# Kernel optimization log

Measured on AMD Instinct MI355X. Metric: run time of the kernel, lower is better.

## Reference

```python
import jax, jax.numpy as jnp
import numpy as np

B, S, D = 2, 2048, 1024
H, DK = 16, 64          # heads, d_k (= d_v)
DH = 4096               # FFN hidden
EPS = 1e-5


def _layer_norm(x, gamma, beta):
    mu = jnp.mean(x, axis=-1, keepdims=True)
    var = jnp.var(x, axis=-1, keepdims=True)
    return (x - mu) * jax.lax.rsqrt(var + EPS) * gamma + beta


def setup_inputs() -> dict:
    key = jax.random.key(0)
    ks = jax.random.split(key, 8)
    s = lambda fan_in: 1.0 / np.sqrt(fan_in)
    return {
        "x": jax.random.normal(ks[0], (B, S, D), dtype=jnp.float32),
        # NOTE: source module uses W_q for queries, keys AND values (bug kept faithfully),
        # so W_k / W_v are never used and are not materialized.
        "Wq": jax.random.normal(ks[1], (D, H * DK), dtype=jnp.float32) * s(D),
        "bq": jnp.zeros((H * DK,), dtype=jnp.float32),
        "Wo": jax.random.normal(ks[2], (H * DK, D), dtype=jnp.float32) * s(H * DK),
        "bo": jnp.zeros((D,), dtype=jnp.float32),
        "ln1_g": jnp.ones((D,), dtype=jnp.float32),
        "ln1_b": jnp.zeros((D,), dtype=jnp.float32),
        "W1": jax.random.normal(ks[3], (D, DH), dtype=jnp.float32) * s(D),
        "b1": jnp.zeros((DH,), dtype=jnp.float32),
        "W2": jax.random.normal(ks[4], (DH, D), dtype=jnp.float32) * s(DH),
        "b2": jnp.zeros((D,), dtype=jnp.float32),
        "ln2_g": jnp.ones((D,), dtype=jnp.float32),
        "ln2_b": jnp.zeros((D,), dtype=jnp.float32),
    }


def reference(x, Wq, bq, Wo, bo, ln1_g, ln1_b, W1, b1, W2, b2, ln2_g, ln2_b):
    residual = x
    # projections: q, k, v all use W_q (faithful to source)
    q = (x @ Wq + bq).reshape(B, S, H, DK)
    k = (x @ Wq + bq).reshape(B, S, H, DK)
    v = (x @ Wq + bq).reshape(B, S, H, DK)
    # scores scaled by sqrt(sequence_length), as in the source
    scale = 1.0 / jnp.sqrt(jnp.float32(S))
    scores = jnp.einsum("bqhd,bkhd->bhqk", q, k) * scale
    probs = jax.nn.softmax(scores, axis=-1)
    attn = jnp.einsum("bhqk,bkhd->bqhd", probs, v).reshape(B, S, H * DK)
    attn = attn @ Wo + bo
    # dropout is identity in eval mode
    x = _layer_norm(attn + residual, ln1_g, ln1_b)
    residual = x
    h = jax.nn.relu(x @ W1 + b1)
    x = h @ W2 + b2
    x = _layer_norm(x + residual, ln2_g, ln2_b)
    return x
```

## Files before the change

kernel.cpp:

```cpp
#include <hip/hip_runtime.h>
#include <stdint.h>


typedef unsigned short u16;
typedef __attribute__((ext_vector_type(8))) short v8s;
typedef __attribute__((ext_vector_type(4))) float v4f;

#define AS1 __attribute__((address_space(1)))
#define AS3 __attribute__((address_space(3)))

__device__ __forceinline__ void gl_lds16(const u16* g, u16* l) {
  __builtin_amdgcn_global_load_lds((const AS1 void*)g, (AS3 void*)l, 16, 0, 0);
}

__device__ __forceinline__ float bf2f(u16 u) {
  union { uint32_t i; float f; } v; v.i = ((uint32_t)u) << 16; return v.f;
}
__device__ __forceinline__ u16 f2bf(float f) {
  union { float f; uint32_t i; } v; v.f = f;
  uint32_t x = v.i;
  return (u16)((x + 0x7FFFu + ((x >> 16) & 1u)) >> 16);
}
__device__ __forceinline__ uint32_t fbits(float f) {
  union { float f; uint32_t u; } v; v.f = f; return v.u;
}

__global__ __launch_bounds__(256) void cvt_f2b(
    const float* __restrict__ src, u16* __restrict__ dst, int n4) {
  int i = (blockIdx.x * 256 + threadIdx.x);
  if (i < n4) {
    float4 v = *(const float4*)(src + (size_t)i * 4);
    ushort4 o;
    o.x = f2bf(v.x); o.y = f2bf(v.y); o.z = f2bf(v.z); o.w = f2bf(v.w);
    *(ushort4*)(dst + (size_t)i * 4) = o;
  }
}

__global__ __launch_bounds__(256) void transpose_f2b(
    const float* __restrict__ src, u16* __restrict__ dst,
    int R, int C, int ld_s, int ld_d) {
  __shared__ float tile[32][33];
  const int tx = threadIdx.x & 31, ty = threadIdx.x >> 5;
  const int c0 = blockIdx.x * 32, r0 = blockIdx.y * 32;
#pragma unroll
  for (int j = 0; j < 32; j += 8)
    tile[ty + j][tx] = src[(size_t)(r0 + ty + j) * ld_s + c0 + tx];
  __syncthreads();
#pragma unroll
  for (int j = 0; j < 32; j += 8)
    dst[(size_t)(c0 + ty + j) * ld_d + r0 + tx] = f2bf(tile[tx][ty + j]);
}

__global__ __launch_bounds__(256) void transpose_b2b(
    const u16* __restrict__ src, u16* __restrict__ dst,
    int R, int C, int ld_s, int ld_d) {
  __shared__ u16 tile[32][33];
  const int tx = threadIdx.x & 31, ty = threadIdx.x >> 5;
  const int c0 = blockIdx.x * 32, r0 = blockIdx.y * 32;
#pragma unroll
  for (int j = 0; j < 32; j += 8)
    tile[ty + j][tx] = src[(size_t)(r0 + ty + j) * ld_s + c0 + tx];
  __syncthreads();
#pragma unroll
  for (int j = 0; j < 32; j += 8)
    dst[(size_t)(c0 + ty + j) * ld_d + r0 + tx] = tile[tx][ty + j];
}

__global__ __launch_bounds__(256) void gemm_g1(
    const u16* __restrict__ A, const u16* __restrict__ Bt,
    const float* __restrict__ bias, void* __restrict__ C,
    int M, int N, int ldk, int klen, int relu, int accum, int out_f32,
    int atomic) {
  __shared__ u16 As[2][4096];
  __shared__ u16 Bs[2][4096];
  const int tid = threadIdx.x;
  const int w = tid >> 6, l = tid & 63;
  const int lane16 = l & 15, kgrp = l >> 4;
  const int m0 = blockIdx.y * 128, n0 = blockIdx.x * 128;
  const int k_begin = blockIdx.z * klen;
  const int wr = (w >> 1) * 64, wc = (w & 1) * 64;

  const int sr = w * 32 + (l >> 2);
  const int sc = l & 3;
  const int sgc = sc ^ ((sr & 3) ^ ((sr >> 2) & 3));
  const u16* gA = A + (size_t)(m0 + sr) * ldk + k_begin + 8 * sgc;
  const u16* gB = Bt + (size_t)(n0 + sr) * ldk + k_begin + 8 * sgc;
  const size_t rstep = (size_t)16 * ldk;
  const int fl = (lane16 & 3) ^ ((lane16 >> 2) & 3);

  v4f acc[4][4];
#pragma unroll
  for (int i = 0; i < 4; i++)
#pragma unroll
    for (int j = 0; j < 4; j++)
#pragma unroll
      for (int r = 0; r < 4; r++) acc[i][j][r] = 0.f;

  gl_lds16(gA, &As[0][w * 1024]);
  gl_lds16(gA + rstep, &As[0][w * 1024 + 512]);
  gl_lds16(gB, &Bs[0][w * 1024]);
  gl_lds16(gB + rstep, &Bs[0][w * 1024 + 512]);

  int cur = 0;
  for (int k0 = 0; k0 < klen; k0 += 32) {
    __syncthreads();
    if (k0 + 32 < klen) {
      int nxt = cur ^ 1;
      gl_lds16(gA + k0 + 32, &As[nxt][w * 1024]);
      gl_lds16(gA + k0 + 32 + rstep, &As[nxt][w * 1024 + 512]);
      gl_lds16(gB + k0 + 32, &Bs[nxt][w * 1024]);
      gl_lds16(gB + k0 + 32 + rstep, &Bs[nxt][w * 1024 + 512]);
    }
    v8s a[4], b[4];
#pragma unroll
    for (int mi = 0; mi < 4; mi++)
      a[mi] = *(const v8s*)(&As[cur][(wr + mi * 16 + lane16) * 32 + 8 * (kgrp ^ fl)]);
#pragma unroll
    for (int ni = 0; ni < 4; ni++)
      b[ni] = *(const v8s*)(&Bs[cur][(wc + ni * 16 + lane16) * 32 + 8 * (kgrp ^ fl)]);
#pragma unroll
    for (int mi = 0; mi < 4; mi++)
#pragma unroll
      for (int ni = 0; ni < 4; ni++)
        acc[mi][ni] = __builtin_amdgcn_mfma_f32_16x16x32_bf16(a[mi], b[ni], acc[mi][ni], 0, 0, 0);
    cur ^= 1;
  }

#pragma unroll
  for (int ni = 0; ni < 4; ni++) {
    int col = n0 + wc + ni * 16 + lane16;
    float bv = (bias && k_begin == 0) ? bias[col] : 0.f;
#pragma unroll
    for (int mi = 0; mi < 4; mi++) {
      int row = m0 + wr + mi * 16 + kgrp * 4;
#pragma unroll
      for (int r = 0; r < 4; r++) {
        float v = acc[mi][ni][r] + bv;
        if (relu) v = fmaxf(v, 0.f);
        size_t idx = (size_t)(row + r) * N + col;
        if (atomic) {
          atomicAdd(&((float*)C)[idx], v);
        } else if (out_f32) {
          float* Cf = (float*)C;
          if (accum) v += Cf[idx];
          Cf[idx] = v;
        } else {
          ((u16*)C)[idx] = f2bf(v);
        }
      }
    }
  }
}

__global__ __launch_bounds__(256) void gemm_g2(
    const u16* __restrict__ A, const u16* __restrict__ Bt,
    const float* __restrict__ bias, void* __restrict__ C,
    int M, int N, int K, int relu, int accum, int out_f32) {
  __shared__ u16 As[2][8192];
  __shared__ u16 Bs[2][4096];
  const int tid = threadIdx.x;
  const int w = tid >> 6, l = tid & 63;
  const int l16 = l & 15, kgrp = l >> 4;
  const int m0 = blockIdx.y * 128, n0 = blockIdx.x * 64;
  const int wr = (w >> 1) * 64, wc = (w & 1) * 32;

  const int srow = w * 8 + (l >> 3);
  const u16* gA[4];
#pragma unroll
  for (int i = 0; i < 4; i++) {
    int r = i * 32 + srow;
    gA[i] = A + (size_t)(m0 + r) * K + 8 * ((l & 7) ^ (r & 7));
  }
  const u16* gB[2];
#pragma unroll
  for (int i = 0; i < 2; i++) {
    int r = i * 32 + srow;
    gB[i] = Bt + (size_t)(n0 + r) * K + 8 * ((l & 7) ^ (r & 7));
  }

  v4f acc[4][2];
#pragma unroll
  for (int i = 0; i < 4; i++)
#pragma unroll
    for (int j = 0; j < 2; j++)
#pragma unroll
      for (int r = 0; r < 4; r++) acc[i][j][r] = 0.f;

#pragma unroll
  for (int i = 0; i < 4; i++) gl_lds16(gA[i], &As[0][(i * 256 + w * 64) * 8]);
#pragma unroll
  for (int i = 0; i < 2; i++) gl_lds16(gB[i], &Bs[0][(i * 256 + w * 64) * 8]);

  int cur = 0;
  for (int k0 = 0; k0 < K; k0 += 64) {
    __syncthreads();
    if (k0 + 64 < K) {
      int nxt = cur ^ 1;
#pragma unroll
      for (int i = 0; i < 4; i++)
        gl_lds16(gA[i] + k0 + 64, &As[nxt][(i * 256 + w * 64) * 8]);
#pragma unroll
      for (int i = 0; i < 2; i++)
        gl_lds16(gB[i] + k0 + 64, &Bs[nxt][(i * 256 + w * 64) * 8]);
    }
    v8s a[4][2], b[2][2];
#pragma unroll
    for (int ks = 0; ks < 2; ks++) {
      int ch = 8 * ((ks * 4 + kgrp) ^ (l16 & 7));
#pragma unroll
      for (int mi = 0; mi < 4; mi++)
        a[mi][ks] = *(const v8s*)(&As[cur][(wr + mi * 16 + l16) * 64 + ch]);
#pragma unroll
      for (int ni = 0; ni < 2; ni++)
        b[ni][ks] = *(const v8s*)(&Bs[cur][(wc + ni * 16 + l16) * 64 + ch]);
    }
#pragma unroll
    for (int ks = 0; ks < 2; ks++)
#pragma unroll
      for (int mi = 0; mi < 4; mi++)
#pragma unroll
        for (int ni = 0; ni < 2; ni++)
          acc[mi][ni] = __builtin_amdgcn_mfma_f32_16x16x32_bf16(a[mi][ks], b[ni][ks], acc[mi][ni], 0, 0, 0);
    cur ^= 1;
  }

#pragma unroll
  for (int ni = 0; ni < 2; ni++) {
    int col = n0 + wc + ni * 16 + l16;
    float bv = bias ? bias[col] : 0.f;
#pragma unroll
    for (int mi = 0; mi < 4; mi++) {
      int row = m0 + wr + mi * 16 + kgrp * 4;
#pragma unroll
      for (int r = 0; r < 4; r++) {
        float v = acc[mi][ni][r] + bv;
        if (relu) v = fmaxf(v, 0.f);
        size_t idx = (size_t)(row + r) * N + col;
        if (out_f32) {
          float* Cf = (float*)C;
          if (accum) v += Cf[idx];
          Cf[idx] = v;
        } else {
          ((u16*)C)[idx] = f2bf(v);
        }
      }
    }
  }
}

__global__ __launch_bounds__(256) void attn_kernel(
    const u16* __restrict__ Q, const u16* __restrict__ Qt,
    u16* __restrict__ O) {
  __shared__ u16 KV[2][8192];
  __shared__ __align__(16) u16 Ps[4][2304];
  const int tid = threadIdx.x;
  const int w = tid >> 6, l = tid & 63;
  const int l16 = l & 15, kgrp = l >> 4;
  const int bh = blockIdx.y, b = bh >> 4, h = bh & 15;
  const int q0 = blockIdx.x * 128;
  const size_t rowQ = (size_t)(b * 2048 + q0 + w * 32);
  const float cexp = 1.4426950408889634f / 45.254833995939045f;

  const int srow = w * 8 + (l >> 3);
  const int sch8 = 8 * ((l & 7) ^ (srow & 7));
  const u16* gK0 = Q + (size_t)(b * 2048 + srow) * 1024 + h * 64 + sch8;
  const u16* gK1 = gK0 + (size_t)32 * 1024;
  const u16* gV0 = Qt + (size_t)(h * 64 + srow) * 4096 + b * 2048 + sch8;
  const u16* gV1 = gV0 + (size_t)32 * 4096;

  v8s qb[2][2];
#pragma unroll
  for (int nj = 0; nj < 2; nj++)
#pragma unroll
    for (int ks = 0; ks < 2; ks++) {
      v8s t = *(const v8s*)(Q + (rowQ + nj * 16 + l16) * 1024 + h * 64 + ks * 32 + kgrp * 8);
#pragma unroll
      for (int j = 0; j < 8; j++) t[j] = (short)f2bf(bf2f((u16)t[j]) * cexp);
      qb[nj][ks] = t;
    }

  v4f o[2][4];
  float ls[2] = {0.f, 0.f};
#pragma unroll
  for (int i = 0; i < 2; i++)
#pragma unroll
    for (int j = 0; j < 4; j++)
#pragma unroll
      for (int r = 0; r < 4; r++) o[i][j][r] = 0.f;

  gl_lds16(gK0, &KV[0][w * 512]);
  gl_lds16(gK1, &KV[0][2048 + w * 512]);
  gl_lds16(gV0, &KV[0][4096 + w * 512]);
  gl_lds16(gV1, &KV[0][4096 + 2048 + w * 512]);

  u16* Pw = &Ps[w][0];
  int cur = 0;
  for (int kb = 0; kb < 2048; kb += 64) {
    __syncthreads();
    if (kb + 64 < 2048) {
      int nxt = cur ^ 1;
      gl_lds16(gK0 + (size_t)(kb + 64) * 1024, &KV[nxt][w * 512]);
      gl_lds16(gK1 + (size_t)(kb + 64) * 1024, &KV[nxt][2048 + w * 512]);
      gl_lds16(gV0 + (kb + 64), &KV[nxt][4096 + w * 512]);
      gl_lds16(gV1 + (kb + 64), &KV[nxt][4096 + 2048 + w * 512]);
    }
    const u16* Ks = &KV[cur][0];
    const u16* Vt = &KV[cur][4096];

    v4f st[4][2];
#pragma unroll
    for (int i = 0; i < 4; i++)
#pragma unroll
      for (int j = 0; j < 2; j++)
#pragma unroll
        for (int r = 0; r < 4; r++) st[i][j][r] = 0.f;
#pragma unroll
    for (int ks = 0; ks < 2; ks++) {
      v8s ka[4];
#pragma unroll
      for (int mi = 0; mi < 4; mi++)
        ka[mi] = *(const v8s*)(Ks + (mi * 16 + l16) * 64 + 8 * ((ks * 4 + kgrp) ^ (l16 & 7)));
#pragma unroll
      for (int mi = 0; mi < 4; mi++)
#pragma unroll
        for (int nj = 0; nj < 2; nj++)
          st[mi][nj] = __builtin_amdgcn_mfma_f32_16x16x32_bf16(ka[mi], qb[nj][ks], st[mi][nj], 0, 0, 0);
    }

#pragma unroll
    for (int mi = 0; mi < 4; mi++)
#pragma unroll
      for (int nj = 0; nj < 2; nj++) {
        float p0 = __builtin_amdgcn_exp2f(st[mi][nj][0]);
        float p1 = __builtin_amdgcn_exp2f(st[mi][nj][1]);
        float p2 = __builtin_amdgcn_exp2f(st[mi][nj][2]);
        float p3 = __builtin_amdgcn_exp2f(st[mi][nj][3]);
        ls[nj] += (p0 + p1) + (p2 + p3);
        uint2 pk;
        pk.x = __builtin_amdgcn_perm(fbits(p1), fbits(p0), 0x07060302u);
        pk.y = __builtin_amdgcn_perm(fbits(p3), fbits(p2), 0x07060302u);
        *(uint2*)(Pw + (nj * 16 + l16) * 72 + mi * 16 + kgrp * 4) = pk;
      }

#pragma unroll
    for (int t = 0; t < 2; t++) {
      v8s pa[2], vb[4];
#pragma unroll
      for (int nj = 0; nj < 2; nj++)
        pa[nj] = *(const v8s*)(Pw + (nj * 16 + l16) * 72 + t * 32 + kgrp * 8);
#pragma unroll
      for (int ni = 0; ni < 4; ni++)
        vb[ni] = *(const v8s*)(Vt + (ni * 16 + l16) * 64 + 8 * ((t * 4 + kgrp) ^ (l16 & 7)));
#pragma unroll
      for (int nj = 0; nj < 2; nj++)
#pragma unroll
        for (int ni = 0; ni < 4; ni++)
          o[nj][ni] = __builtin_amdgcn_mfma_f32_16x16x32_bf16(pa[nj], vb[ni], o[nj][ni], 0, 0, 0);
    }
    cur ^= 1;
  }

#pragma unroll
  for (int nj = 0; nj < 2; nj++) {
    float t = ls[nj];
    t += __shfl_xor(t, 16, 64);
    t += __shfl_xor(t, 32, 64);
    ls[nj] = t;
  }

#pragma unroll
  for (int nj = 0; nj < 2; nj++) {
#pragma unroll
    for (int r = 0; r < 4; r++) {
      float den = __shfl(ls[nj], kgrp * 4 + r, 64);
      float rden = 1.f / den;
#pragma unroll
      for (int ni = 0; ni < 4; ni++) {
        O[(rowQ + nj * 16 + kgrp * 4 + r) * 1024 + h * 64 + ni * 16 + l16] =
            f2bf(o[nj][ni][r] * rden);
      }
    }
  }
}

__global__ __launch_bounds__(256) void ln_residual(
    const void* __restrict__ Y, const void* __restrict__ Xr,
    const float* __restrict__ g, const float* __restrict__ bb,
    void* __restrict__ out, int yf, int xf, int of) {
  const int row = blockIdx.x, tid = threadIdx.x;
  const size_t base = (size_t)row * 1024;
  float v[4], s = 0.f, sq = 0.f;
#pragma unroll
  for (int i = 0; i < 4; i++) {
    int c = tid + i * 256;
    float ya = yf ? ((const float*)Y)[base + c] : bf2f(((const u16*)Y)[base + c]);
    float xa = xf ? ((const float*)Xr)[base + c] : bf2f(((const u16*)Xr)[base + c]);
    float x = ya + xa;
    v[i] = x; s += x; sq += x * x;
  }
#pragma unroll
  for (int off = 32; off >= 1; off >>= 1) {
    s += __shfl_down(s, off, 64);
    sq += __shfl_down(sq, off, 64);
  }
  __shared__ float rs[4], rq[4];
  const int w = tid >> 6, l = tid & 63;
  if (l == 0) { rs[w] = s; rq[w] = sq; }
  __syncthreads();
  s = rs[0] + rs[1] + rs[2] + rs[3];
  sq = rq[0] + rq[1] + rq[2] + rq[3];
  const float mu = s * (1.f / 1024.f);
  const float var = sq * (1.f / 1024.f) - mu * mu;
  const float rstd = rsqrtf(var + 1e-5f);
#pragma unroll
  for (int i = 0; i < 4; i++) {
    int c = tid + i * 256;
    float r = (v[i] - mu) * rstd * g[c] + bb[c];
    if (of) ((float*)out)[base + c] = r;
    else ((u16*)out)[base + c] = f2bf(r);
  }
}

extern "C" void kernel_launch(void* const* d_in, const int* in_sizes, int n_in,
                              void* d_out, int out_size, void* d_ws, size_t ws_size,
                              hipStream_t stream) {
  const float* x   = (const float*)d_in[0];
  const float* Wq  = (const float*)d_in[1];
  const float* bq  = (const float*)d_in[2];
  const float* Wo  = (const float*)d_in[3];
  const float* bo  = (const float*)d_in[4];
  const float* g1  = (const float*)d_in[5];
  const float* be1 = (const float*)d_in[6];
  const float* W1  = (const float*)d_in[7];
  const float* b1  = (const float*)d_in[8];
  const float* W2  = (const float*)d_in[9];
  const float* b2  = (const float*)d_in[10];
  const float* g2  = (const float*)d_in[11];
  const float* be2 = (const float*)d_in[12];
  float* out = (float*)d_out;
  u16* ws  = (u16*)d_ws;

  const size_t M1 = 1048576;
  dim3 blk(256);
  const bool big = ws_size >= (size_t)37 * M1 * 2;

  if (big) {
    u16* xb   = ws + 0;
    u16* Qb   = ws + 4 * M1;
    u16* Qt   = ws + 8 * M1;
    u16* WqT  = ws + 12 * M1;
    u16* W1T  = ws + 13 * M1;
    u16* W2T  = ws + 17 * M1;
    u16* Hh   = ws + 21 * M1;
    u16* attn = xb;  u16* Yb = Qt;  u16* x1 = Qb;  u16* WoT = WqT;

    hipMemsetAsync(out, 0, (size_t)out_size * sizeof(float), stream);

    cvt_f2b<<<dim3(4096), blk, 0, stream>>>(x, xb, 1048576);
    transpose_f2b<<<dim3(32, 32), blk, 0, stream>>>(Wq, WqT, 1024, 1024, 1024, 1024);
    gemm_g2<<<dim3(16, 32), blk, 0, stream>>>(xb, WqT, bq, Qb, 4096, 1024, 1024, 0, 0, 0);

    transpose_b2b<<<dim3(32, 128), blk, 0, stream>>>(Qb, Qt, 4096, 1024, 1024, 4096);
    attn_kernel<<<dim3(16, 32), blk, 0, stream>>>(Qb, Qt, attn);

    transpose_f2b<<<dim3(32, 32), blk, 0, stream>>>(Wo, WoT, 1024, 1024, 1024, 1024);
    gemm_g2<<<dim3(16, 32), blk, 0, stream>>>(attn, WoT, bo, Yb, 4096, 1024, 1024, 0, 0, 0);
    ln_residual<<<dim3(4096), blk, 0, stream>>>(Yb, x, g1, be1, x1, 0, 1, 0);

    transpose_f2b<<<dim3(128, 32), blk, 0, stream>>>(W1, W1T, 1024, 4096, 4096, 1024);
    gemm_g1<<<dim3(32, 32, 1), blk, 0, stream>>>(x1, W1T, b1, Hh, 4096, 4096,
                                                 1024, 1024, 1, 0, 0, 0);
    transpose_f2b<<<dim3(32, 128), blk, 0, stream>>>(W2, W2T, 4096, 1024, 1024, 4096);
    gemm_g1<<<dim3(8, 32, 4), blk, 0, stream>>>(Hh, W2T, b2, out, 4096, 1024,
                                                4096, 1024, 0, 0, 1, 1);

    ln_residual<<<dim3(4096), blk, 0, stream>>>(out, x1, g2, be2, out, 1, 0, 1);
  } else {
    u16* xb   = ws + 0;
    u16* Qb   = ws + 4 * M1;
    u16* Qt   = ws + 8 * M1;
    u16* attn = xb;  u16* Yb = Qt;  u16* x1 = Qb;  u16* Hc = xb;
    u16* Wt1  = ws + 12 * M1;
    u16* Wt2  = ws + 13 * M1;

    cvt_f2b<<<dim3(4096), blk, 0, stream>>>(x, xb, 1048576);
    transpose_f2b<<<dim3(32, 32), blk, 0, stream>>>(Wq, Wt1, 1024, 1024, 1024, 1024);
    gemm_g2<<<dim3(16, 32), blk, 0, stream>>>(xb, Wt1, bq, Qb, 4096, 1024, 1024, 0, 0, 0);

    transpose_b2b<<<dim3(32, 128), blk, 0, stream>>>(Qb, Qt, 4096, 1024, 1024, 4096);
    attn_kernel<<<dim3(16, 32), blk, 0, stream>>>(Qb, Qt, attn);

    transpose_f2b<<<dim3(32, 32), blk, 0, stream>>>(Wo, Wt2, 1024, 1024, 1024, 1024);
    gemm_g2<<<dim3(16, 32), blk, 0, stream>>>(attn, Wt2, bo, Yb, 4096, 1024, 1024, 0, 0, 0);
    ln_residual<<<dim3(4096), blk, 0, stream>>>(Yb, x, g1, be1, x1, 0, 1, 0);

    for (int c = 0; c < 4; c++) {
      transpose_f2b<<<dim3(32, 32), blk, 0, stream>>>(W1 + (size_t)c * 1024, Wt1,
                                                      1024, 1024, 4096, 1024);
      gemm_g2<<<dim3(16, 32), blk, 0, stream>>>(x1, Wt1, b1 + (size_t)c * 1024, Hc,
                                                4096, 1024, 1024, 1, 0, 0);
      transpose_f2b<<<dim3(32, 32), blk, 0, stream>>>(W2 + (size_t)c * M1, Wt2,
                                                      1024, 1024, 1024, 1024);
      gemm_g2<<<dim3(16, 32), blk, 0, stream>>>(Hc, Wt2, (c == 0) ? b2 : (const float*)nullptr,
                                                out, 4096, 1024, 1024, 0, (c > 0) ? 1 : 0, 1);
    }
    ln_residual<<<dim3(4096), blk, 0, stream>>>(out, x1, g2, be2, out, 1, 0, 1);
  }
}
```

Before: 391.4 us.

## Replace atomic split-K with two-way split-K partial buffers reduced in LayerNorm

Adds a split-K GEMM variant (gemm_g2s) that writes the first K-half to the main output and the second K-half as bf16 partials to a scratch buffer. The LayerNorm kernel now sums the two partials, which removes the memset and the fp32 atomicAdd reduction in the W2 GEMM. Split-K is also applied to the Wo projection to raise block count. The trade-off is extra partial-buffer traffic, and storing the second partial in bf16 costs some precision.

```diff
diff --git a/kernel.cpp b/kernel.cpp
--- a/kernel.cpp
+++ b/kernel.cpp
@@ -69,23 +69,21 @@
 __global__ __launch_bounds__(256) void gemm_g1(
     const u16* __restrict__ A, const u16* __restrict__ Bt,
     const float* __restrict__ bias, void* __restrict__ C,
-    int M, int N, int ldk, int klen, int relu, int accum, int out_f32,
-    int atomic) {
+    int M, int N, int K, int relu, int out_f32) {
   __shared__ u16 As[2][4096];
   __shared__ u16 Bs[2][4096];
   const int tid = threadIdx.x;
   const int w = tid >> 6, l = tid & 63;
   const int lane16 = l & 15, kgrp = l >> 4;
   const int m0 = blockIdx.y * 128, n0 = blockIdx.x * 128;
-  const int k_begin = blockIdx.z * klen;
   const int wr = (w >> 1) * 64, wc = (w & 1) * 64;
 
   const int sr = w * 32 + (l >> 2);
   const int sc = l & 3;
   const int sgc = sc ^ ((sr & 3) ^ ((sr >> 2) & 3));
-  const u16* gA = A + (size_t)(m0 + sr) * ldk + k_begin + 8 * sgc;
-  const u16* gB = Bt + (size_t)(n0 + sr) * ldk + k_begin + 8 * sgc;
-  const size_t rstep = (size_t)16 * ldk;
+  const u16* gA = A + (size_t)(m0 + sr) * K + 8 * sgc;
+  const u16* gB = Bt + (size_t)(n0 + sr) * K + 8 * sgc;
+  const size_t rstep = (size_t)16 * K;
   const int fl = (lane16 & 3) ^ ((lane16 >> 2) & 3);
 
   v4f acc[4][4];
@@ -102,9 +100,9 @@
   gl_lds16(gB + rstep, &Bs[0][w * 1024 + 512]);
 
   int cur = 0;
-  for (int k0 = 0; k0 < klen; k0 += 32) {
+  for (int k0 = 0; k0 < K; k0 += 32) {
     __syncthreads();
-    if (k0 + 32 < klen) {
+    if (k0 + 32 < K) {
       int nxt = cur ^ 1;
       gl_lds16(gA + k0 + 32, &As[nxt][w * 1024]);
       gl_lds16(gA + k0 + 32 + rstep, &As[nxt][w * 1024 + 512]);
@@ -129,7 +127,7 @@
 #pragma unroll
   for (int ni = 0; ni < 4; ni++) {
     int col = n0 + wc + ni * 16 + lane16;
-    float bv = (bias && k_begin == 0) ? bias[col] : 0.f;
+    float bv = bias ? bias[col] : 0.f;
 #pragma unroll
     for (int mi = 0; mi < 4; mi++) {
       int row = m0 + wr + mi * 16 + kgrp * 4;
@@ -138,15 +136,8 @@
         float v = acc[mi][ni][r] + bv;
         if (relu) v = fmaxf(v, 0.f);
         size_t idx = (size_t)(row + r) * N + col;
-        if (atomic) {
-          atomicAdd(&((float*)C)[idx], v);
-        } else if (out_f32) {
-          float* Cf = (float*)C;
-          if (accum) v += Cf[idx];
-          Cf[idx] = v;
-        } else {
-          ((u16*)C)[idx] = f2bf(v);
-        }
+        if (out_f32) ((float*)C)[idx] = v;
+        else ((u16*)C)[idx] = f2bf(v);
       }
     }
   }
@@ -248,6 +239,102 @@
   }
 }
 
+__global__ __launch_bounds__(256) void gemm_g2s(
+    const u16* __restrict__ A, const u16* __restrict__ Bt,
+    const float* __restrict__ bias, void* __restrict__ C0,
+    u16* __restrict__ C1, int M, int N, int ldk, int klen, int c0_f32) {
+  __shared__ u16 As[2][8192];
+  __shared__ u16 Bs[2][4096];
+  const int tid = threadIdx.x;
+  const int w = tid >> 6, l = tid & 63;
+  const int l16 = l & 15, kgrp = l >> 4;
+  const int m0 = blockIdx.y * 128, n0 = blockIdx.x * 64;
+  const int z = blockIdx.z;
+  const int k_begin = z * klen;
+  const int wr = (w >> 1) * 64, wc = (w & 1) * 32;
+
+  const int srow = w * 8 + (l >> 3);
+  const u16* gA[4];
+#pragma unroll
+  for (int i = 0; i < 4; i++) {
+    int r = i * 32 + srow;
+    gA[i] = A + (size_t)(m0 + r) * ldk + k_begin + 8 * ((l & 7) ^ (r & 7));
+  }
+  const u16* gB[2];
+#pragma unroll
+  for (int i = 0; i < 2; i++) {
+    int r = i * 32 + srow;
+    gB[i] = Bt + (size_t)(n0 + r) * ldk + k_begin + 8 * ((l & 7) ^ (r & 7));
+  }
+
+  v4f acc[4][2];
+#pragma unroll
+  for (int i = 0; i < 4; i++)
+#pragma unroll
+    for (int j = 0; j < 2; j++)
+#pragma unroll
+      for (int r = 0; r < 4; r++) acc[i][j][r] = 0.f;
+
+#pragma unroll
+  for (int i = 0; i < 4; i++) gl_lds16(gA[i], &As[0][(i * 256 + w * 64) * 8]);
+#pragma unroll
+  for (int i = 0; i < 2; i++) gl_lds16(gB[i], &Bs[0][(i * 256 + w * 64) * 8]);
+
+  int cur = 0;
+  for (int k0 = 0; k0 < klen; k0 += 64) {
+    __syncthreads();
+    if (k0 + 64 < klen) {
+      int nxt = cur ^ 1;
+#pragma unroll
+      for (int i = 0; i < 4; i++)
+        gl_lds16(gA[i] + k0 + 64, &As[nxt][(i * 256 + w * 64) * 8]);
+#pragma unroll
+      for (int i = 0; i < 2; i++)
+        gl_lds16(gB[i] + k0 + 64, &Bs[nxt][(i * 256 + w * 64) * 8]);
+    }
+    v8s a[4][2], b[2][2];
+#pragma unroll
+    for (int ks = 0; ks < 2; ks++) {
+      int ch = 8 * ((ks * 4 + kgrp) ^ (l16 & 7));
+#pragma unroll
+      for (int mi = 0; mi < 4; mi++)
+        a[mi][ks] = *(const v8s*)(&As[cur][(wr + mi * 16 + l16) * 64 + ch]);
+#pragma unroll
+      for (int ni = 0; ni < 2; ni++)
+        b[ni][ks] = *(const v8s*)(&Bs[cur][(wc + ni * 16 + l16) * 64 + ch]);
+    }
+#pragma unroll
+    for (int ks = 0; ks < 2; ks++)
+#pragma unroll
+      for (int mi = 0; mi < 4; mi++)
+#pragma unroll
+        for (int ni = 0; ni < 2; ni++)
+          acc[mi][ni] = __builtin_amdgcn_mfma_f32_16x16x32_bf16(a[mi][ks], b[ni][ks], acc[mi][ni], 0, 0, 0);
+    cur ^= 1;
+  }
+
+#pragma unroll
+  for (int ni = 0; ni < 2; ni++) {
+    int col = n0 + wc + ni * 16 + l16;
+    float bv = (bias && z == 0) ? bias[col] : 0.f;
+#pragma unroll
+    for (int mi = 0; mi < 4; mi++) {
+      int row = m0 + wr + mi * 16 + kgrp * 4;
+#pragma unroll
+      for (int r = 0; r < 4; r++) {
+        float v = acc[mi][ni][r] + bv;
+        size_t idx = (size_t)(row + r) * N + col;
+        if (z == 0) {
+          if (c0_f32) ((float*)C0)[idx] = v;
+          else ((u16*)C0)[idx] = f2bf(v);
+        } else {
+          C1[idx] = f2bf(v);
+        }
+      }
+    }
+  }
+}
+
 __global__ __launch_bounds__(256) void attn_kernel(
     const u16* __restrict__ Q, const u16* __restrict__ Qt,
     u16* __restrict__ O) {
@@ -384,9 +471,10 @@
 }
 
 __global__ __launch_bounds__(256) void ln_residual(
-    const void* __restrict__ Y, const void* __restrict__ Xr,
+    const void* __restrict__ Y, const void* __restrict__ Y2,
+    const void* __restrict__ Xr,
     const float* __restrict__ g, const float* __restrict__ bb,
-    void* __restrict__ out, int yf, int xf, int of) {
+    void* __restrict__ out, int yf, int y2f, int xf, int of) {
   const int row = blockIdx.x, tid = threadIdx.x;
   const size_t base = (size_t)row * 1024;
   float v[4], s = 0.f, sq = 0.f;
@@ -396,6 +484,10 @@
     float ya = yf ? ((const float*)Y)[base + c] : bf2f(((const u16*)Y)[base + c]);
     float xa = xf ? ((const float*)Xr)[base + c] : bf2f(((const u16*)Xr)[base + c]);
     float x = ya + xa;
+    if (Y2) {
+      float y2a = y2f ? ((const float*)Y2)[base + c] : bf2f(((const u16*)Y2)[base + c]);
+      x += y2a;
+    }
     v[i] = x; s += x; sq += x * x;
   }
 #pragma unroll
@@ -453,8 +545,8 @@
     u16* W2T  = ws + 17 * M1;
     u16* Hh   = ws + 21 * M1;
     u16* attn = xb;  u16* Yb = Qt;  u16* x1 = Qb;  u16* WoT = WqT;
-
-    hipMemsetAsync(out, 0, (size_t)out_size * sizeof(float), stream);
+    u16* P1wo = W1T;
+    u16* P1f2 = Qt;
 
     cvt_f2b<<<dim3(4096), blk, 0, stream>>>(x, xb, 1048576);
     transpose_f2b<<<dim3(32, 32), blk, 0, stream>>>(Wq, WqT, 1024, 1024, 1024, 1024);
@@ -464,17 +556,18 @@
     attn_kernel<<<dim3(16, 32), blk, 0, stream>>>(Qb, Qt, attn);
 
     transpose_f2b<<<dim3(32, 32), blk, 0, stream>>>(Wo, WoT, 1024, 1024, 1024, 1024);
-    gemm_g2<<<dim3(16, 32), blk, 0, stream>>>(attn, WoT, bo, Yb, 4096, 1024, 1024, 0, 0, 0);
-    ln_residual<<<dim3(4096), blk, 0, stream>>>(Yb, x, g1, be1, x1, 0, 1, 0);
+    gemm_g2s<<<dim3(16, 32, 2), blk, 0, stream>>>(attn, WoT, bo, Yb, P1wo,
+                                                  4096, 1024, 1024, 512, 0);
+    ln_residual<<<dim3(4096), blk, 0, stream>>>(Yb, P1wo, x, g1, be1, x1, 0, 0, 1, 0);
 
     transpose_f2b<<<dim3(128, 32), blk, 0, stream>>>(W1, W1T, 1024, 4096, 4096, 1024);
-    gemm_g1<<<dim3(32, 32, 1), blk, 0, stream>>>(x1, W1T, b1, Hh, 4096, 4096,
-                                                 1024, 1024, 1, 0, 0, 0);
+    gemm_g1<<<dim3(32, 32), blk, 0, stream>>>(x1, W1T, b1, Hh, 4096, 4096, 1024, 1, 0);
+
     transpose_f2b<<<dim3(32, 128), blk, 0, stream>>>(W2, W2T, 4096, 1024, 1024, 4096);
-    gemm_g1<<<dim3(8, 32, 4), blk, 0, stream>>>(Hh, W2T, b2, out, 4096, 1024,
-                                                4096, 1024, 0, 0, 1, 1);
-
-    ln_residual<<<dim3(4096), blk, 0, stream>>>(out, x1, g2, be2, out, 1, 0, 1);
+    gemm_g2s<<<dim3(16, 32, 2), blk, 0, stream>>>(Hh, W2T, b2, out, P1f2,
+                                                  4096, 1024, 4096, 2048, 1);
+
+    ln_residual<<<dim3(4096), blk, 0, stream>>>(out, P1f2, x1, g2, be2, out, 1, 0, 0, 1);
   } else {
     u16* xb   = ws + 0;
     u16* Qb   = ws + 4 * M1;
@@ -492,7 +585,7 @@
 
     transpose_f2b<<<dim3(32, 32), blk, 0, stream>>>(Wo, Wt2, 1024, 1024, 1024, 1024);
     gemm_g2<<<dim3(16, 32), blk, 0, stream>>>(attn, Wt2, bo, Yb, 4096, 1024, 1024, 0, 0, 0);
-    ln_residual<<<dim3(4096), blk, 0, stream>>>(Yb, x, g1, be1, x1, 0, 1, 0);
+    ln_residual<<<dim3(4096), blk, 0, stream>>>(Yb, nullptr, x, g1, be1, x1, 0, 0, 1, 0);
 
     for (int c = 0; c < 4; c++) {
       transpose_f2b<<<dim3(32, 32), blk, 0, stream>>>(W1 + (size_t)c * 1024, Wt1,
@@ -504,6 +597,6 @@
       gemm_g2<<<dim3(16, 32), blk, 0, stream>>>(Hc, Wt2, (c == 0) ? b2 : (const float*)nullptr,
                                                 out, 4096, 1024, 1024, 0, (c > 0) ? 1 : 0, 1);
     }
-    ln_residual<<<dim3(4096), blk, 0, stream>>>(out, x1, g2, be2, out, 1, 0, 1);
-  }
-}
+    ln_residual<<<dim3(4096), blk, 0, stream>>>(out, nullptr, x1, g2, be2, out, 1, 0, 0, 1);
+  }
+}
```

New measurement: 355.9 us. -9.1%, faster.
